# Kernel optimization log

Hardware: AMD Instinct MI355X
Metric: run time of the kernel (lower is better)

The kernel has to match this reference:

```python
import jax, jax.numpy as jnp
from jax import lax
import numpy as np

B, T, I, H, O = 256, 1024, 64, 256, 1


def setup_inputs() -> dict:
    key = jax.random.key(0)
    ks = jax.random.split(key, 7)
    s = 0.05
    return {
        "x": jax.random.normal(ks[0], (B, T, I), dtype=jnp.float32),
        "W_ih": jax.random.normal(ks[1], (4 * H, I), dtype=jnp.float32) * s,
        "W_hh": jax.random.normal(ks[2], (4 * H, H), dtype=jnp.float32) * s,
        "b_ih": jax.random.normal(ks[3], (4 * H,), dtype=jnp.float32) * s,
        "b_hh": jax.random.normal(ks[4], (4 * H,), dtype=jnp.float32) * s,
        "fc_w": jax.random.normal(ks[5], (O, H), dtype=jnp.float32) * s,
        "fc_b": jax.random.normal(ks[6], (O,), dtype=jnp.float32) * s,
    }


def _lstm_last_hidden(x, W_ih, W_hh, b_ih, b_hh):
    # x: [B, T, I] -> last hidden state h_T: [B, H]
    h_dim = W_hh.shape[1]
    xT = jnp.swapaxes(x, 0, 1)                      # [T, B, I]
    # Precompute input contribution to gates for all timesteps (one big GEMM)
    x_gates = jnp.einsum("tbi,gi->tbg", xT, W_ih) + b_ih + b_hh  # [T, B, 4H]

    def step(carry, xg):
        h, c = carry
        g = xg + h @ W_hh.T                         # [B, 4H]
        i, f, gg, o = jnp.split(g, 4, axis=-1)       # torch gate order i,f,g,o
        i = jax.nn.sigmoid(i)
        f = jax.nn.sigmoid(f)
        gg = jnp.tanh(gg)
        o = jax.nn.sigmoid(o)
        c = f * c + i * gg
        h = o * jnp.tanh(c)
        return (h, c), None

    b = x.shape[0]
    h0 = jnp.zeros((b, h_dim), dtype=x.dtype)
    c0 = jnp.zeros((b, h_dim), dtype=x.dtype)
    (h_last, _), _ = lax.scan(step, (h0, c0), x_gates)
    return h_last


def reference(x, W_ih, W_hh, b_ih, b_hh, fc_w, fc_b):
    h_last = _lstm_last_hidden(x, W_ih, W_hh, b_ih, b_hh)  # [B, H]
    return h_last @ fc_w.T + fc_b                           # [B, O]
```

## Files before the change

kernel.cpp:

```cpp
#include <hip/hip_runtime.h>
#include <stdint.h>


#define T_ 1024
#define I_ 64
#define H_ 256
#define NSLICE 8
#define NGROUP 32
#define MB 8
#define HB 32
#define HROW 272

#define UNITS_PER_GROUP 1024
#define UNITS_PER_PARITY (NGROUP * UNITS_PER_GROUP)
#define SENT_CAP (1 << 16)

typedef float floatx4 __attribute__((ext_vector_type(4)));
typedef __bf16 bf16x8 __attribute__((ext_vector_type(8)));
typedef unsigned short ushortx8 __attribute__((ext_vector_type(8)));
typedef unsigned int uintx4 __attribute__((ext_vector_type(4)));
typedef unsigned int uint32;
typedef unsigned long long u64;

__device__ __forceinline__ float bf2f(uint32 u16) {
  uint32 u = u16 << 16;
  return __builtin_bit_cast(float, u);
}
__device__ __forceinline__ unsigned short f2bf(float f) {
  uint32 u = __builtin_bit_cast(uint32, f);
  u = (u + 0x7FFFu + ((u >> 16) & 1u)) >> 16;
  return (unsigned short)u;
}
__device__ __forceinline__ bf16x8 packbf8(floatx4 a, floatx4 b) {
  bf16x8 r;
  r[0] = (__bf16)a[0]; r[1] = (__bf16)a[1];
  r[2] = (__bf16)a[2]; r[3] = (__bf16)a[3];
  r[4] = (__bf16)b[0]; r[5] = (__bf16)b[1];
  r[6] = (__bf16)b[2]; r[7] = (__bf16)b[3];
  return r;
}
__device__ __forceinline__ float fast_sig(float v) {
  return 1.0f / (1.0f + __expf(-v));
}
__device__ __forceinline__ float fast_tanh(float v) {
  float e = __expf(2.0f * v);
  return 1.0f - 2.0f / (e + 1.0f);
}
__device__ __forceinline__ u64 aload64(const u64* p) {
  return __hip_atomic_load(p, __ATOMIC_RELAXED, __HIP_MEMORY_SCOPE_AGENT);
}

__global__ __launch_bounds__(256, 1) void lstm_main(
    const float* __restrict__ x, const float* __restrict__ W_ih,
    const float* __restrict__ W_hh, const float* __restrict__ b_ih,
    const float* __restrict__ b_hh, u64* __restrict__ units) {
  const int tid = threadIdx.x;
  const int bid = blockIdx.x;
  const int s = bid >> 5;
  const int g = bid & 31;
  const int w = tid >> 6;
  const int lane = tid & 63;
  const int ln = lane & 15;
  const int lk = lane >> 4;

  __shared__ float xch[4][2][16][8];
  __shared__ __align__(16) unsigned short h_lds[MB][HROW];

  {
    uint32* p = (uint32*)&h_lds[0][0];
    for (int i = tid; i < MB * HROW / 2; i += 256) p[i] = 0u;
  }

  bf16x8 wf[2][10];
  float bias[2];
#pragma unroll
  for (int j = 0; j < 2; ++j) {
    const int row = w * 256 + s * HB + j * 16 + ln;
    bias[j] = b_ih[row] + b_hh[row];
#pragma unroll
    for (int kc = 0; kc < 10; ++kc) {
      const int kk = kc * 32 + lk * 8;
      const float* src = (kk < I_) ? (W_ih + (size_t)row * I_ + kk)
                                   : (W_hh + (size_t)row * H_ + (kk - I_));
      floatx4 f0 = *(const floatx4*)src;
      floatx4 f1 = *(const floatx4*)(src + 4);
      wf[j][kc] = packbf8(f0, f1);
    }
  }

  const int mb = ln & 7;
  const float* xrow = x + ((size_t)(g * MB + mb)) * T_ * I_;
  const int um = tid >> 5;
  const int uh = tid & 31;
  const int uj = uh >> 4, un = uh & 15;
  float c_reg = 0.0f;

  const size_t gbase = (size_t)g * UNITS_PER_GROUP;

  __syncthreads();

#pragma unroll 1
  for (int t = 0; t < T_; ++t) {
    floatx4 xf0, xf1, xf2, xf3;
    {
      const float* src = xrow + t * I_ + lk * 8;
      xf0 = *(const floatx4*)(src);
      xf1 = *(const floatx4*)(src + 4);
      xf2 = *(const floatx4*)(src + 32);
      xf3 = *(const floatx4*)(src + 36);
    }

    if (t > 0) {
      const u64* up =
          units + (size_t)(t & 1) * UNITS_PER_PARITY + gbase + tid * 4;
      u64 v0 = aload64(up + 0);
      u64 v1 = aload64(up + 1);
      u64 v2 = aload64(up + 2);
      u64 v3 = aload64(up + 3);
      bool ok = ((uint32)(v0 >> 32) == (uint32)t) &
                ((uint32)(v1 >> 32) == (uint32)t) &
                ((uint32)(v2 >> 32) == (uint32)t) &
                ((uint32)(v3 >> 32) == (uint32)t);
      int it = 0;
      while (!__all(ok) && ++it < SENT_CAP) {
        __builtin_amdgcn_s_sleep(1);
        if (!ok) {
          v0 = aload64(up + 0);
          v1 = aload64(up + 1);
          v2 = aload64(up + 2);
          v3 = aload64(up + 3);
          ok = ((uint32)(v0 >> 32) == (uint32)t) &
               ((uint32)(v1 >> 32) == (uint32)t) &
               ((uint32)(v2 >> 32) == (uint32)t) &
               ((uint32)(v3 >> 32) == (uint32)t);
        }
      }
      uintx4 d;
      d[0] = (uint32)v0; d[1] = (uint32)v1;
      d[2] = (uint32)v2; d[3] = (uint32)v3;
      uint32* dst = (uint32*)&h_lds[tid >> 5][0] + (tid & 31) * 4;
      *(uintx4*)dst = d;
    }
    __syncthreads();

    bf16x8 af[10];
    af[0] = packbf8(xf0, xf1);
    af[1] = packbf8(xf2, xf3);
    const unsigned short* hrow = &h_lds[mb][0];
#pragma unroll
    for (int kc = 2; kc < 10; ++kc) {
      af[kc] =
          __builtin_bit_cast(bf16x8, *(const ushortx8*)(hrow + (kc - 2) * 32 +
                                                        lk * 8));
    }

    floatx4 acc[2];
    acc[0] = (floatx4){bias[0], bias[0], bias[0], bias[0]};
    acc[1] = (floatx4){bias[1], bias[1], bias[1], bias[1]};
#pragma unroll
    for (int kc = 0; kc < 10; ++kc) {
      acc[0] = __builtin_amdgcn_mfma_f32_16x16x32_bf16(af[kc], wf[0][kc],
                                                       acc[0], 0, 0, 0);
      acc[1] = __builtin_amdgcn_mfma_f32_16x16x32_bf16(af[kc], wf[1][kc],
                                                       acc[1], 0, 0, 0);
    }

#pragma unroll
    for (int j = 0; j < 2; ++j) {
      floatx4 v = acc[j];
      if (w == 2) {
        v[0] = fast_tanh(v[0]); v[1] = fast_tanh(v[1]);
        v[2] = fast_tanh(v[2]); v[3] = fast_tanh(v[3]);
      } else {
        v[0] = fast_sig(v[0]); v[1] = fast_sig(v[1]);
        v[2] = fast_sig(v[2]); v[3] = fast_sig(v[3]);
      }
      if (lk < 2) {
        *(floatx4*)&xch[w][j][ln][lk * 4] = v;
      }
    }
    __syncthreads();

    float ig = xch[0][uj][un][um];
    float fg = xch[1][uj][un][um];
    float gg = xch[2][uj][un][um];
    float og = xch[3][uj][un][um];
    c_reg = fg * c_reg + ig * gg;
    float hv = og * fast_tanh(c_reg);

    unsigned short hb = __builtin_bit_cast(unsigned short, (__bf16)hv);
    int pv = __shfl_xor((int)hb, 1);
    if ((uh & 1) == 0) {
      uint32 dword = (uint32)hb | ((uint32)(unsigned short)pv << 16);
      u64 val = (u64)dword | ((u64)(uint32)(t + 1) << 32);
      u64* dst = units + (size_t)((t + 1) & 1) * UNITS_PER_PARITY + gbase +
                 (um * 128 + s * 16 + (uh >> 1));
      __hip_atomic_store(dst, val, __ATOMIC_RELAXED,
                         __HIP_MEMORY_SCOPE_AGENT);
    }
  }
}

__global__ void lstm_fc(const u64* __restrict__ units,
                        const float* __restrict__ fc_w,
                        const float* __restrict__ fc_b,
                        float* __restrict__ out) {
  const int b = threadIdx.x;
  const int g = b >> 3, m = b & 7;
  const u64* base = units + (size_t)g * UNITS_PER_GROUP + m * 128;
  float sum = fc_b[0];
#pragma unroll 8
  for (int d = 0; d < 128; ++d) {
    u64 v = aload64(base + d);
    uint32 lo = (uint32)v;
    sum += bf2f(lo & 0xffffu) * fc_w[2 * d] + bf2f(lo >> 16) * fc_w[2 * d + 1];
  }
  out[b] = sum;
}

extern "C" void kernel_launch(void* const* d_in, const int* in_sizes, int n_in,
                              void* d_out, int out_size, void* d_ws,
                              size_t ws_size, hipStream_t stream) {
  const float* x    = (const float*)d_in[0];
  const float* W_ih = (const float*)d_in[1];
  const float* W_hh = (const float*)d_in[2];
  const float* b_ih = (const float*)d_in[3];
  const float* b_hh = (const float*)d_in[4];
  const float* fc_w = (const float*)d_in[5];
  const float* fc_b = (const float*)d_in[6];
  float* out = (float*)d_out;

  u64* units = (u64*)d_ws;

  lstm_main<<<dim3(NGROUP * NSLICE), dim3(256), 0, stream>>>(
      x, W_ih, W_hh, b_ih, b_hh, units);
  lstm_fc<<<dim3(1), dim3(256), 0, stream>>>(units, fc_w, fc_b, out);
}
```

Before: 2.223 ms.

## Halve hidden slices per batch group, doubling per-block hidden width to 64

Each block now owns 64 hidden units per gate instead of 32, so only 4 slices cooperate per batch group and the grid shrinks from 256 to 128 blocks. Each wave issues 4 MFMA chains per step and each thread updates two cell states and publishes two h words. The intent is to reduce cross-block synchronisation and polling traffic per timestep, at the cost of more serial work and register pressure per block on the critical path.

```diff
diff --git a/kernel.cpp b/kernel.cpp
--- a/kernel.cpp
+++ b/kernel.cpp
@@ -5,10 +5,10 @@
 #define T_ 1024
 #define I_ 64
 #define H_ 256
-#define NSLICE 8
+#define NSLICE 4
 #define NGROUP 32
 #define MB 8
-#define HB 32
+#define HB 64
 #define HROW 272
 
 #define UNITS_PER_GROUP 1024
@@ -63,7 +63,7 @@
   const int ln = lane & 15;
   const int lk = lane >> 4;
 
-  __shared__ float xch[4][2][16][8];
+  __shared__ float xch[4][4][16][8];
   __shared__ __align__(16) unsigned short h_lds[MB][HROW];
 
   {
@@ -71,10 +71,10 @@
     for (int i = tid; i < MB * HROW / 2; i += 256) p[i] = 0u;
   }
 
-  bf16x8 wf[2][10];
-  float bias[2];
-#pragma unroll
-  for (int j = 0; j < 2; ++j) {
+  bf16x8 wf[4][10];
+  float bias[4];
+#pragma unroll
+  for (int j = 0; j < 4; ++j) {
     const int row = w * 256 + s * HB + j * 16 + ln;
     bias[j] = b_ih[row] + b_hh[row];
 #pragma unroll
@@ -93,7 +93,7 @@
   const int um = tid >> 5;
   const int uh = tid & 31;
   const int uj = uh >> 4, un = uh & 15;
-  float c_reg = 0.0f;
+  float c0 = 0.0f, c1 = 0.0f;
 
   const size_t gbase = (size_t)g * UNITS_PER_GROUP;
 
@@ -154,19 +154,20 @@
                                                         lk * 8));
     }
 
-    floatx4 acc[2];
-    acc[0] = (floatx4){bias[0], bias[0], bias[0], bias[0]};
-    acc[1] = (floatx4){bias[1], bias[1], bias[1], bias[1]};
+    floatx4 acc[4];
+#pragma unroll
+    for (int j = 0; j < 4; ++j)
+      acc[j] = (floatx4){bias[j], bias[j], bias[j], bias[j]};
 #pragma unroll
     for (int kc = 0; kc < 10; ++kc) {
-      acc[0] = __builtin_amdgcn_mfma_f32_16x16x32_bf16(af[kc], wf[0][kc],
-                                                       acc[0], 0, 0, 0);
-      acc[1] = __builtin_amdgcn_mfma_f32_16x16x32_bf16(af[kc], wf[1][kc],
-                                                       acc[1], 0, 0, 0);
-    }
-
-#pragma unroll
-    for (int j = 0; j < 2; ++j) {
+#pragma unroll
+      for (int j = 0; j < 4; ++j)
+        acc[j] = __builtin_amdgcn_mfma_f32_16x16x32_bf16(af[kc], wf[j][kc],
+                                                         acc[j], 0, 0, 0);
+    }
+
+#pragma unroll
+    for (int j = 0; j < 4; ++j) {
       floatx4 v = acc[j];
       if (w == 2) {
         v[0] = fast_tanh(v[0]); v[1] = fast_tanh(v[1]);
@@ -181,21 +182,32 @@
     }
     __syncthreads();
 
-    float ig = xch[0][uj][un][um];
-    float fg = xch[1][uj][un][um];
-    float gg = xch[2][uj][un][um];
-    float og = xch[3][uj][un][um];
-    c_reg = fg * c_reg + ig * gg;
-    float hv = og * fast_tanh(c_reg);
-
-    unsigned short hb = __builtin_bit_cast(unsigned short, (__bf16)hv);
-    int pv = __shfl_xor((int)hb, 1);
+    float ig0 = xch[0][uj][un][um];
+    float fg0 = xch[1][uj][un][um];
+    float gg0 = xch[2][uj][un][um];
+    float og0 = xch[3][uj][un][um];
+    float ig1 = xch[0][uj + 2][un][um];
+    float fg1 = xch[1][uj + 2][un][um];
+    float gg1 = xch[2][uj + 2][un][um];
+    float og1 = xch[3][uj + 2][un][um];
+    c0 = fg0 * c0 + ig0 * gg0;
+    float h0 = og0 * fast_tanh(c0);
+    c1 = fg1 * c1 + ig1 * gg1;
+    float h1 = og1 * fast_tanh(c1);
+
+    unsigned short hb0 = __builtin_bit_cast(unsigned short, (__bf16)h0);
+    unsigned short hb1 = __builtin_bit_cast(unsigned short, (__bf16)h1);
+    int pv0 = __shfl_xor((int)hb0, 1);
+    int pv1 = __shfl_xor((int)hb1, 1);
     if ((uh & 1) == 0) {
-      uint32 dword = (uint32)hb | ((uint32)(unsigned short)pv << 16);
-      u64 val = (u64)dword | ((u64)(uint32)(t + 1) << 32);
-      u64* dst = units + (size_t)((t + 1) & 1) * UNITS_PER_PARITY + gbase +
-                 (um * 128 + s * 16 + (uh >> 1));
-      __hip_atomic_store(dst, val, __ATOMIC_RELAXED,
+      u64* base = units + (size_t)((t + 1) & 1) * UNITS_PER_PARITY + gbase +
+                  (um * 128 + s * 32 + (uh >> 1));
+      uint32 d0 = (uint32)hb0 | ((uint32)(unsigned short)pv0 << 16);
+      uint32 d1 = (uint32)hb1 | ((uint32)(unsigned short)pv1 << 16);
+      u64 tag = ((u64)(uint32)(t + 1) << 32);
+      __hip_atomic_store(base, (u64)d0 | tag, __ATOMIC_RELAXED,
+                         __HIP_MEMORY_SCOPE_AGENT);
+      __hip_atomic_store(base + 16, (u64)d1 | tag, __ATOMIC_RELAXED,
                          __HIP_MEMORY_SCOPE_AGENT);
     }
   }
```

Result: slower. 2.586 ms (+16.3%).
